# Kernel tuning notes

Hardware: AMD Instinct MI355X
Metric: run time of the kernel (lower is better)

## Reference

```python
import jax, jax.numpy as jnp
import numpy as np

N = 100000          # nodes
E = 1600000         # edges
D_IN = 128
HID = 256
N_CLASSES = 10
N_GRAPHS = 64


def gcn_conv(x, src, dst, W, b, n_nodes):
    """PyG GCNConv: add self-loops, symmetric deg^{-1/2} normalization, x@W, scatter-add."""
    h = x @ W  # [N, out]
    loop = jnp.arange(n_nodes, dtype=src.dtype)
    src2 = jnp.concatenate([src, loop])
    dst2 = jnp.concatenate([dst, loop])
    deg = jax.ops.segment_sum(jnp.ones(src2.shape[0], x.dtype), dst2, num_segments=n_nodes)
    dinv = jax.lax.rsqrt(deg)  # deg >= 1 thanks to self-loops
    norm = dinv[src2] * dinv[dst2]  # [E+N]
    msg = norm[:, None] * h[src2]   # [E+N, out]
    return jax.ops.segment_sum(msg, dst2, num_segments=n_nodes) + b


def setup_inputs() -> dict:
    key = jax.random.key(0)
    ks = jax.random.split(key, 12)
    x = jax.random.normal(ks[0], (N, D_IN), dtype=jnp.float32)
    edge_index = jax.random.randint(ks[1], (2, E), 0, N, dtype=jnp.int64)
    batch = jnp.sort(jax.random.randint(ks[2], (N,), 0, N_GRAPHS, dtype=jnp.int64))
    def glorot(k, shape):
        lim = float(np.sqrt(6.0 / (shape[0] + shape[1])))
        return jax.random.uniform(k, shape, jnp.float32, -lim, lim)
    W1 = glorot(ks[3], (D_IN, HID));  b1 = jnp.zeros((HID,), jnp.float32)
    W2 = glorot(ks[4], (HID, HID));   b2 = jnp.zeros((HID,), jnp.float32)
    Wf1 = glorot(ks[5], (HID, HID));  bf1 = jnp.zeros((HID,), jnp.float32)
    Wf2 = glorot(ks[6], (HID, N_CLASSES)); bf2 = jnp.zeros((N_CLASSES,), jnp.float32)
    return {"x": x, "edge_index": edge_index, "batch": batch,
            "W1": W1, "b1": b1, "W2": W2, "b2": b2,
            "Wf1": Wf1, "bf1": bf1, "Wf2": Wf2, "bf2": bf2}


def reference(x, edge_index, batch, W1, b1, W2, b2, Wf1, bf1, Wf2, bf2):
    src, dst = edge_index[0], edge_index[1]
    h = jax.nn.relu(gcn_conv(x, src, dst, W1, b1, N))
    h = jax.nn.relu(gcn_conv(h, src, dst, W2, b2, N))
    # global mean pool over graph ids
    summed = jax.ops.segment_sum(h, batch, num_segments=N_GRAPHS)  # [G, HID]
    counts = jax.ops.segment_sum(jnp.ones((N,), h.dtype), batch, num_segments=N_GRAPHS)
    pooled = summed / jnp.maximum(counts, 1.0)[:, None]
    z = jax.nn.relu(pooled @ Wf1 + bf1)
    alpha = jax.nn.softplus(z @ Wf2 + bf2) + 0.001
    return alpha
```

## Files before the change

kernel.cpp:

```cpp
#include <hip/hip_runtime.h>
#include <math.h>

#define NN   100000
#define NE   1600000
#define DIN  128
#define HID  256
#define NG   64
#define NCLS 10

#define NBLK 128
#define EPB  (NE / NBLK)
#define NBUK 512
#define NPB  196

using bf16x8 = __attribute__((ext_vector_type(8))) short;
using f32x4  = __attribute__((ext_vector_type(4))) float;
using f32x2  = __attribute__((ext_vector_type(2))) float;
using u32x2  = __attribute__((ext_vector_type(2))) unsigned int;

static __device__ __forceinline__ unsigned short f2bf(float f) {
    unsigned u = __float_as_uint(f);
    u += 0x7fff + ((u >> 16) & 1);
    return (unsigned short)(u >> 16);
}
static __device__ __forceinline__ float bf2f(unsigned short h) {
    return __uint_as_float(((unsigned)h) << 16);
}

static __device__ __forceinline__ unsigned char f32_to_fp8(float f) {
    float a = fminf(fabsf(f), 448.f);
    unsigned bits = __float_as_uint(a * 0x1p-120f);
    bits += 0x7ffff + ((bits >> 20) & 1);
    unsigned e4 = (bits >> 20) & 0x7f;
    return (unsigned char)(e4 | (f < 0.f ? 0x80u : 0u));
}
#if __has_builtin(__builtin_amdgcn_cvt_pk_f32_fp8)
#define HAVE_CVT_FP8 1
#endif
static __device__ __forceinline__ void fp8x4_to_f32(unsigned u, float* f) {
#ifdef HAVE_CVT_FP8
    f32x2 lo = __builtin_amdgcn_cvt_pk_f32_fp8((int)u, false);
    f32x2 hi = __builtin_amdgcn_cvt_pk_f32_fp8((int)u, true);
    f[0] = lo[0]; f[1] = lo[1]; f[2] = hi[0]; f[3] = hi[1];
#else
#pragma unroll
    for (int k = 0; k < 4; ++k) {
        unsigned b = (u >> (8 * k)) & 0xffu;
        unsigned bits = ((b & 0x80u) << 24) | ((b & 0x7fu) << 20);
        f[k] = __uint_as_float(bits) * 0x1p+120f;
    }
#endif
}


__global__ __launch_bounds__(256) void k_hist(const int* __restrict__ dst,
                                              int* __restrict__ histg) {
    __shared__ int h[NBUK];
    const int t = threadIdx.x;
    for (int i = t; i < NBUK; i += 256) h[i] = 0;
    __syncthreads();
    const int e0 = blockIdx.x * EPB, e1 = e0 + EPB;
    for (int e = e0 + t; e < e1; e += 256)
        atomicAdd(&h[(unsigned)__builtin_nontemporal_load(&dst[e]) / NPB], 1);
    __syncthreads();
    for (int i = t; i < NBUK; i += 256)
        histg[i * NBLK + blockIdx.x] = h[i];
}

__global__ __launch_bounds__(1024) void k_scan64k(int* __restrict__ d) {
    __shared__ int ts[1024];
    const int t = threadIdx.x;
    const int base = t * 64;
    int s = 0;
    for (int i = 0; i < 64; ++i) s += d[base + i];
    ts[t] = s;
    __syncthreads();
    for (int off = 1; off < 1024; off <<= 1) {
        int u = (t >= off) ? ts[t - off] : 0;
        __syncthreads();
        ts[t] += u;
        __syncthreads();
    }
    int run = ts[t] - s;
    for (int i = 0; i < 64; ++i) {
        int v = d[base + i];
        d[base + i] = run;
        run += v;
    }
}

__global__ __launch_bounds__(256) void k_scatter(const int* __restrict__ src,
                                                 const int* __restrict__ dst,
                                                 const int* __restrict__ offg,
                                                 int2* __restrict__ pairs) {
    __shared__ int cur[NBUK];
    const int t = threadIdx.x;
    for (int i = t; i < NBUK; i += 256) cur[i] = offg[i * NBLK + blockIdx.x];
    __syncthreads();
    const int e0 = blockIdx.x * EPB, e1 = e0 + EPB;
    for (int e = e0 + t; e < e1; e += 256) {
        int d = __builtin_nontemporal_load(&dst[e]);
        int sv = __builtin_nontemporal_load(&src[e]);
        int b = (unsigned)d / NPB;
        int p = atomicAdd(&cur[b], 1);
        u32x2 pv; pv.x = (unsigned)sv; pv.y = (unsigned)d;
        __builtin_nontemporal_store(pv, (u32x2*)&pairs[p]);
    }
}

__global__ __launch_bounds__(256) void k_csr(const int2* __restrict__ pairs,
                                             const int* __restrict__ offg,
                                             int* __restrict__ csr,
                                             int* __restrict__ deg,
                                             float* __restrict__ dinv,
                                             int* __restrict__ offs) {
    __shared__ int cnt[NPB];
    __shared__ int loff[256];
    __shared__ int cur[NPB];
    const int b = blockIdx.x, t = threadIdx.x;
    const int s     = offg[b * NBLK];
    const int e_end = (b == NBUK - 1) ? NE : offg[(b + 1) * NBLK];
    const int nb0   = b * NPB;
    const int nnod  = min(NPB, NN - nb0);
    if (t < NPB) cnt[t] = 0;
    __syncthreads();
    for (int e = s + t; e < e_end; e += 256)
        atomicAdd(&cnt[pairs[e].y - nb0], 1);
    __syncthreads();
    int v = (t < NPB) ? cnt[t] : 0;
    loff[t] = v;
    __syncthreads();
    for (int off = 1; off < 256; off <<= 1) {
        int u = (t >= off) ? loff[t - off] : 0;
        __syncthreads();
        loff[t] += u;
        __syncthreads();
    }
    int myoff = loff[t] - v;
    __syncthreads();
    loff[t] = myoff;
    if (t < NPB) cur[t] = 0;
    __syncthreads();
    if (t < nnod) {
        int node = nb0 + t;
        int dg = cnt[t];
        deg[node]  = dg;
        dinv[node] = rsqrtf((float)(dg + 1));
        offs[node] = s + myoff;
    }
    for (int e = s + t; e < e_end; e += 256) {
        int2 pr = pairs[e];
        int li = pr.y - nb0;
        int p = atomicAdd(&cur[li], 1);
        csr[s + loff[li] + p] = pr.x;
    }
}

__global__ void k_counts(const int* __restrict__ batch, float* __restrict__ countsf) {
    int g = threadIdx.x;
    if (g >= NG) return;
    int lo = 0, hi = NN;
    while (lo < hi) { int mid = (lo + hi) >> 1; if (batch[mid] < g) lo = mid + 1; else hi = mid; }
    int lb = lo;
    lo = 0; hi = NN;
    while (lo < hi) { int mid = (lo + hi) >> 1; if (batch[mid] <= g) lo = mid + 1; else hi = mid; }
    countsf[g] = (float)(lo - lb);
}


__global__ void k_cast_scale_x(const float* __restrict__ x, const float* __restrict__ dinv,
                               unsigned short* __restrict__ xb, int n4) {
    int i = blockIdx.x * blockDim.x + threadIdx.x;
    if (i >= n4) return;
    float dv = dinv[i >> 5];
    const float4 v = *(const float4*)&x[i * 4];
    ushort4 o;
    o.x = f2bf(v.x * dv); o.y = f2bf(v.y * dv);
    o.z = f2bf(v.z * dv); o.w = f2bf(v.w * dv);
    *(ushort4*)&xb[i * 4] = o;
}

__global__ void k_cast_wt2(const float* __restrict__ W1, unsigned short* __restrict__ Wt1,
                           const float* __restrict__ W2, unsigned short* __restrict__ Wt2) {
    int i = blockIdx.x * blockDim.x + threadIdx.x;
    if (i < DIN * HID) {
        int k = i >> 8, nc = i & 255;
        Wt1[nc * DIN + k] = f2bf(W1[i]);
    } else if (i < (DIN + HID) * HID) {
        int j = i - DIN * HID;
        int k = j >> 8, nc = j & 255;
        Wt2[nc * HID + k] = f2bf(W2[j]);
    }
}


template <int MODE>
__global__ __launch_bounds__(256) void k_gemm_mfma(const unsigned short* __restrict__ A,
                                                   const unsigned short* __restrict__ Wt,
                                                   const float* __restrict__ dinv,
                                                   const float* __restrict__ bias,
                                                   void* __restrict__ outp,
                                                   const int* __restrict__ batch,
                                                   float* __restrict__ pooled,
                                                   int M, int K) {
    __shared__ unsigned short As[128 * 40];
    __shared__ unsigned short Bs[128 * 40];
    __shared__ float psum[4][128];
    __shared__ int gloc[128];
    const int t = threadIdx.x;
    const int lane = t & 63;
    const int wid = t >> 6;
    const int wr = wid >> 1, wc = wid & 1;
    const int bm = blockIdx.x * 128, bn = blockIdx.y * 128;
    const int lr = lane & 15;
    const int ko = (lane >> 4) << 3;

    f32x4 acc[4][4] = {};

    const int r = t >> 2;
    const int kq = (t & 3) << 3;

    int g0 = 0;
    if (MODE == 2) {
        g0 = batch[bm];
        for (int i = t; i < 4 * 128; i += 256) ((float*)psum)[i] = 0.f;
        if (t < 128) gloc[t] = (bm + t < M) ? (batch[bm + t] - g0) : 0;
    }

    for (int kk = 0; kk < K; kk += 32) {
#pragma unroll
        for (int h = 0; h < 128; h += 64) {
            int row = bm + r + h;
            int4 v = make_int4(0, 0, 0, 0);
            if (row < M) v = *(const int4*)&A[(size_t)row * K + kk + kq];
            *(int4*)&As[(r + h) * 40 + kq] = v;
        }
#pragma unroll
        for (int h = 0; h < 128; h += 64) {
            int nrow = bn + r + h;
            int4 v = *(const int4*)&Wt[(size_t)nrow * K + kk + kq];
            *(int4*)&Bs[(r + h) * 40 + kq] = v;
        }
        __syncthreads();
        bf16x8 af[4], bfr[4];
#pragma unroll
        for (int mf = 0; mf < 4; ++mf)
            af[mf] = *(const bf16x8*)&As[(wr * 64 + mf * 16 + lr) * 40 + ko];
#pragma unroll
        for (int nf = 0; nf < 4; ++nf)
            bfr[nf] = *(const bf16x8*)&Bs[(wc * 64 + nf * 16 + lr) * 40 + ko];
#pragma unroll
        for (int mf = 0; mf < 4; ++mf)
#pragma unroll
            for (int nf = 0; nf < 4; ++nf)
                acc[mf][nf] = __builtin_amdgcn_mfma_f32_16x16x32_bf16(af[mf], bfr[nf], acc[mf][nf], 0, 0, 0);
        __syncthreads();
    }

    if (MODE == 1) {
        unsigned char* out8 = (unsigned char*)outp;
#pragma unroll
        for (int mf = 0; mf < 4; ++mf) {
#pragma unroll
            for (int b = 0; b < 4; ++b) {
                int row = bm + wr * 64 + mf * 16 + (lane >> 4) * 4 + b;
                if (row >= M) continue;
                float dv = dinv[row];
#pragma unroll
                for (int nf = 0; nf < 4; ++nf) {
                    int col = bn + wc * 64 + nf * 16 + lr;
                    float v = fmaxf(acc[mf][nf][b] + bias[col], 0.f);
                    out8[(size_t)row * HID + col] = f32_to_fp8(dv * v);
                }
            }
        }
    } else {
        const int q4 = (lane >> 4) << 2;
#pragma unroll
        for (int nf = 0; nf < 4; ++nf) {
            const int lcol = wc * 64 + nf * 16 + lr;
            const float bb = bias[bn + lcol];
            float run = 0.f; int gcur = 0;
#pragma unroll
            for (int mf = 0; mf < 4; ++mf) {
#pragma unroll
                for (int b = 0; b < 4; ++b) {
                    int lrow = wr * 64 + mf * 16 + q4 + b;
                    if (bm + lrow < M) {
                        int gl = gloc[lrow];
                        float v = fmaxf(acc[mf][nf][b] + bb, 0.f);
                        if (gl != gcur) {
                            if (run != 0.f) {
                                if (gcur < 4) atomicAdd(&psum[gcur][lcol], run);
                                else atomicAdd(&pooled[(size_t)(g0 + gcur) * HID + bn + lcol], run);
                            }
                            run = 0.f; gcur = gl;
                        }
                        run += v;
                    }
                }
            }
            if (run != 0.f) {
                if (gcur < 4) atomicAdd(&psum[gcur][lcol], run);
                else atomicAdd(&pooled[(size_t)(g0 + gcur) * HID + bn + lcol], run);
            }
        }
        __syncthreads();
        for (int i = t; i < 4 * 128; i += 256) {
            int gl = i >> 7, lcol = i & 127;
            int g = g0 + gl;
            float v = psum[gl][lcol];
            if (g < NG && v != 0.f)
                atomicAdd(&pooled[(size_t)g * HID + bn + lcol], v);
        }
    }
}


__global__ __launch_bounds__(256) void k_agg256(const unsigned char* __restrict__ hs,
                                                const int* __restrict__ csr,
                                                const int* __restrict__ offs,
                                                const int* __restrict__ deg,
                                                const float* __restrict__ dinv,
                                                unsigned short* __restrict__ out, int n) {
    int wid = threadIdx.x >> 6, lane = threadIdx.x & 63;
    int node = blockIdx.x * 4 + wid;
    if (node >= n) return;
    int c = lane << 2;
    float a0, a1, a2, a3;
    {
        unsigned u = *(const unsigned*)&hs[(size_t)node * HID + c];
        float f[4]; fp8x4_to_f32(u, f);
        a0 = f[0]; a1 = f[1]; a2 = f[2]; a3 = f[3];
    }
    int s0 = offs[node], cnt = deg[node];
    for (int base = 0; base < cnt; base += 64) {
        int nb = min(64, cnt - base);
        int idx = (lane < nb) ? __builtin_nontemporal_load(&csr[s0 + base + lane]) : 0;
        int i = 0;
        for (; i + 8 <= nb; i += 8) {
            unsigned v[8];
#pragma unroll
            for (int k = 0; k < 8; ++k) {
                int j = __shfl(idx, i + k);
                v[k] = *(const unsigned*)&hs[(size_t)j * HID + c];
            }
#pragma unroll
            for (int k = 0; k < 8; ++k) {
                float f[4]; fp8x4_to_f32(v[k], f);
                a0 += f[0]; a1 += f[1]; a2 += f[2]; a3 += f[3];
            }
        }
        for (; i + 4 <= nb; i += 4) {
            unsigned v[4];
#pragma unroll
            for (int k = 0; k < 4; ++k) {
                int j = __shfl(idx, i + k);
                v[k] = *(const unsigned*)&hs[(size_t)j * HID + c];
            }
#pragma unroll
            for (int k = 0; k < 4; ++k) {
                float f[4]; fp8x4_to_f32(v[k], f);
                a0 += f[0]; a1 += f[1]; a2 += f[2]; a3 += f[3];
            }
        }
        for (; i < nb; ++i) {
            int j = __shfl(idx, i);
            unsigned u = *(const unsigned*)&hs[(size_t)j * HID + c];
            float f[4]; fp8x4_to_f32(u, f);
            a0 += f[0]; a1 += f[1]; a2 += f[2]; a3 += f[3];
        }
    }
    float dv = dinv[node];
    ushort4 r;
    r.x = f2bf(dv * a0); r.y = f2bf(dv * a1);
    r.z = f2bf(dv * a2); r.w = f2bf(dv * a3);
    *(ushort4*)&out[(size_t)node * HID + c] = r;
}


__global__ __launch_bounds__(256) void k_agg128(const unsigned short* __restrict__ xs,
                                                const int* __restrict__ csr,
                                                const int* __restrict__ offs,
                                                const int* __restrict__ deg,
                                                const float* __restrict__ dinv,
                                                unsigned short* __restrict__ out, int n) {
    int wid = threadIdx.x >> 6, lane = threadIdx.x & 63;
    int node = blockIdx.x * 4 + wid;
    if (node >= n) return;
    int half = lane >> 5, l32 = lane & 31;
    int c = l32 << 2;
    float a0 = 0.f, a1 = 0.f, a2 = 0.f, a3 = 0.f;
    if (half == 0) {
        const ushort4 s = *(const ushort4*)&xs[(size_t)node * DIN + c];
        a0 = bf2f(s.x); a1 = bf2f(s.y); a2 = bf2f(s.z); a3 = bf2f(s.w);
    }
    int s0 = offs[node], cnt = deg[node];
    for (int base = 0; base < cnt; base += 64) {
        int nb = min(64, cnt - base);
        int idx = (lane < nb) ? __builtin_nontemporal_load(&csr[s0 + base + lane]) : 0;
        int i = 0;
        for (; i + 8 <= nb; i += 8) {
            ushort4 v[4];
#pragma unroll
            for (int k = 0; k < 4; ++k) {
                int j = __shfl(idx, i + 2 * k + half);
                v[k] = *(const ushort4*)&xs[(size_t)j * DIN + c];
            }
#pragma unroll
            for (int k = 0; k < 4; ++k) {
                a0 += bf2f(v[k].x); a1 += bf2f(v[k].y);
                a2 += bf2f(v[k].z); a3 += bf2f(v[k].w);
            }
        }
        for (; i < nb; i += 2) {
            int e = i + half;
            int j = __shfl(idx, e < nb ? e : 0);
            if (e < nb) {
                const ushort4 v = *(const ushort4*)&xs[(size_t)j * DIN + c];
                a0 += bf2f(v.x); a1 += bf2f(v.y); a2 += bf2f(v.z); a3 += bf2f(v.w);
            }
        }
    }
    a0 += __shfl_xor(a0, 32);
    a1 += __shfl_xor(a1, 32);
    a2 += __shfl_xor(a2, 32);
    a3 += __shfl_xor(a3, 32);
    if (half == 0) {
        float dv = dinv[node];
        ushort4 r;
        r.x = f2bf(dv * a0); r.y = f2bf(dv * a1);
        r.z = f2bf(dv * a2); r.w = f2bf(dv * a3);
        *(ushort4*)&out[(size_t)node * DIN + c] = r;
    }
}


__global__ __launch_bounds__(256) void k_mlp(const float* __restrict__ pooled,
                                             const float* __restrict__ countsf,
                                             const float* __restrict__ Wf1,
                                             const float* __restrict__ bf1,
                                             const float* __restrict__ Wf2,
                                             const float* __restrict__ bf2,
                                             float* __restrict__ out) {
    __shared__ float p[HID];
    __shared__ float z[HID];
    int g = blockIdx.x, t = threadIdx.x;
    float cnt = fmaxf(countsf[g], 1.0f);
    p[t] = pooled[g * HID + t] / cnt;
    __syncthreads();
    float accz = bf1[t];
    for (int k = 0; k < HID; ++k)
        accz = fmaf(p[k], Wf1[k * HID + t], accz);
    z[t] = fmaxf(accz, 0.f);
    __syncthreads();
    if (t < NCLS) {
        float o = bf2[t];
        for (int k = 0; k < HID; ++k)
            o = fmaf(z[k], Wf2[k * NCLS + t], o);
        float sp = fmaxf(o, 0.f) + log1pf(expf(-fabsf(o)));
        out[g * NCLS + t] = sp + 0.001f;
    }
}


extern "C" void kernel_launch(void* const* d_in, const int* in_sizes, int n_in,
                              void* d_out, int out_size, void* d_ws, size_t ws_size,
                              hipStream_t stream) {
    const float* x     = (const float*)d_in[0];
    const int*   ei    = (const int*)d_in[1];
    const int*   batch = (const int*)d_in[2];
    const float* W1    = (const float*)d_in[3];
    const float* b1    = (const float*)d_in[4];
    const float* W2    = (const float*)d_in[5];
    const float* b2    = (const float*)d_in[6];
    const float* Wf1   = (const float*)d_in[7];
    const float* bf1   = (const float*)d_in[8];
    const float* Wf2   = (const float*)d_in[9];
    const float* bf2   = (const float*)d_in[10];
    float* out = (float*)d_out;

    const int* srcv = ei;
    const int* dstv = ei + NE;

    char* p = (char*)d_ws;
    auto take = [&](size_t bytes) -> char* {
        char* q = p; p += (bytes + 255) & ~(size_t)255; return q;
    };
    unsigned short* big0 = (unsigned short*)take((size_t)NN * HID * 2);
    unsigned short* big1 = (unsigned short*)take((size_t)NN * HID * 2);
    unsigned short* xs = big0;
    unsigned short* xa = big0 + (size_t)NN * DIN;
    unsigned char*  h8 = (unsigned char*)big1;
    unsigned short* rB = big0;
    int2* pairs = (int2*)big1;
    unsigned short* wt1  = (unsigned short*)take((size_t)DIN * HID * 2);
    unsigned short* wt2  = (unsigned short*)take((size_t)HID * HID * 2);
    int*   histg   = (int*)take((size_t)NBUK * NBLK * 4);
    int*   deg     = (int*)take((size_t)NN * 4);
    int*   offs    = (int*)take((size_t)NN * 4);
    int*   csr     = (int*)take((size_t)NE * 4);
    float* dinv    = (float*)take((size_t)NN * 4);
    float* pooled  = (float*)take((size_t)NG * HID * 4);
    float* countsf = (float*)take((size_t)NG * 4);

    hipMemsetAsync(pooled, 0, (size_t)NG * HID * 4, stream);

    k_hist<<<NBLK, 256, 0, stream>>>(dstv, histg);
    k_scan64k<<<1, 1024, 0, stream>>>(histg);
    k_scatter<<<NBLK, 256, 0, stream>>>(srcv, dstv, histg, pairs);
    k_csr<<<NBUK, 256, 0, stream>>>(pairs, histg, csr, deg, dinv, offs);
    k_counts<<<1, 64, 0, stream>>>(batch, countsf);

    k_cast_scale_x<<<(NN * DIN / 4 + 255) / 256, 256, 0, stream>>>(x, dinv, xs, NN * DIN / 4);
    k_cast_wt2<<<((DIN + HID) * HID + 255) / 256, 256, 0, stream>>>(W1, wt1, W2, wt2);

    dim3 gg((NN + 127) / 128, HID / 128);
    k_agg128<<<(NN + 3) / 4, 256, 0, stream>>>(xs, csr, offs, deg, dinv, xa, NN);
    k_gemm_mfma<1><<<gg, 256, 0, stream>>>(xa, wt1, dinv, b1, (void*)h8, batch, pooled, NN, DIN);
    k_agg256<<<(NN + 3) / 4, 256, 0, stream>>>(h8, csr, offs, deg, dinv, rB, NN);
    k_gemm_mfma<2><<<gg, 256, 0, stream>>>(rB, wt2, dinv, b2, nullptr, batch, pooled, NN, HID);

    k_mlp<<<NG, 256, 0, stream>>>(pooled, countsf, Wf1, bf1, Wf2, bf2, out);
}
```

Measured before the change: 381.8 us.

## Slice node features into column planes for cache-friendly aggregation gathers

Stores fp8 node features in 8 column planes (16 or 32 bytes per node) and launches aggregation blocks per plane so random neighbour gathers work on a much smaller, cache-resident array. The layer-1 input is also quantized to fp8 instead of bf16 to shrink gather traffic. The GEMM epilogue writes the hidden fp8 output in the planar layout. This trades 8x redundant CSR index reads and narrower per-thread loads, and adds fp8 precision loss on the input, for better L2 hit rates.

Result: slower. 525.7 us (+37.7%).

```diff
diff --git a/kernel.cpp b/kernel.cpp
--- a/kernel.cpp
+++ b/kernel.cpp
@@ -168,16 +168,18 @@
 }
 
 
-__global__ void k_cast_scale_x(const float* __restrict__ x, const float* __restrict__ dinv,
-                               unsigned short* __restrict__ xb, int n4) {
+__global__ void k_cast_x8(const float* __restrict__ x, const float* __restrict__ dinv,
+                          unsigned char* __restrict__ xs8, int nq) {
     int i = blockIdx.x * blockDim.x + threadIdx.x;
-    if (i >= n4) return;
-    float dv = dinv[i >> 5];
-    const float4 v = *(const float4*)&x[i * 4];
-    ushort4 o;
-    o.x = f2bf(v.x * dv); o.y = f2bf(v.y * dv);
-    o.z = f2bf(v.z * dv); o.w = f2bf(v.w * dv);
-    *(ushort4*)&xb[i * 4] = o;
+    if (i >= nq) return;
+    int nd = i >> 5;
+    int q  = i & 31;
+    float dv = dinv[nd];
+    const float4 v = *(const float4*)&x[(size_t)nd * DIN + q * 4];
+    uchar4 o;
+    o.x = f32_to_fp8(v.x * dv); o.y = f32_to_fp8(v.y * dv);
+    o.z = f32_to_fp8(v.z * dv); o.w = f32_to_fp8(v.w * dv);
+    *(uchar4*)&xs8[(size_t)(q >> 2) * NN * 16 + (size_t)nd * 16 + (q & 3) * 4] = o;
 }
 
 __global__ void k_cast_wt2(const float* __restrict__ W1, unsigned short* __restrict__ Wt1,
@@ -270,7 +272,8 @@
                 for (int nf = 0; nf < 4; ++nf) {
                     int col = bn + wc * 64 + nf * 16 + lr;
                     float v = fmaxf(acc[mf][nf][b] + bias[col], 0.f);
-                    out8[(size_t)row * HID + col] = f32_to_fp8(dv * v);
+                    out8[(size_t)(col >> 5) * NN * 32 + (size_t)row * 32 + (col & 31)] =
+                        f32_to_fp8(dv * v);
                 }
             }
         }
@@ -317,122 +320,100 @@
 }
 
 
-__global__ __launch_bounds__(256) void k_agg256(const unsigned char* __restrict__ hs,
-                                                const int* __restrict__ csr,
-                                                const int* __restrict__ offs,
-                                                const int* __restrict__ deg,
-                                                const float* __restrict__ dinv,
-                                                unsigned short* __restrict__ out, int n) {
-    int wid = threadIdx.x >> 6, lane = threadIdx.x & 63;
-    int node = blockIdx.x * 4 + wid;
+__global__ __launch_bounds__(256) void k_agg256s(const unsigned char* __restrict__ h8,
+                                                 const int* __restrict__ csr,
+                                                 const int* __restrict__ offs,
+                                                 const int* __restrict__ deg,
+                                                 const float* __restrict__ dinv,
+                                                 unsigned short* __restrict__ out, int n) {
+    const int s = blockIdx.x & 7, grp = blockIdx.x >> 3;
+    const int t = threadIdx.x;
+    const int node = grp * 32 + (t >> 3);
     if (node >= n) return;
-    int c = lane << 2;
+    const int sub = t & 7;
+    const int c4 = sub * 4;
+    const int lane = t & 63;
+    const int lb = lane & ~7;
+    const unsigned char* plane = h8 + (size_t)s * NN * 32;
+
     float a0, a1, a2, a3;
     {
-        unsigned u = *(const unsigned*)&hs[(size_t)node * HID + c];
+        unsigned u = *(const unsigned*)&plane[(size_t)node * 32 + c4];
         float f[4]; fp8x4_to_f32(u, f);
         a0 = f[0]; a1 = f[1]; a2 = f[2]; a3 = f[3];
     }
-    int s0 = offs[node], cnt = deg[node];
-    for (int base = 0; base < cnt; base += 64) {
-        int nb = min(64, cnt - base);
-        int idx = (lane < nb) ? __builtin_nontemporal_load(&csr[s0 + base + lane]) : 0;
-        int i = 0;
-        for (; i + 8 <= nb; i += 8) {
-            unsigned v[8];
-#pragma unroll
-            for (int k = 0; k < 8; ++k) {
-                int j = __shfl(idx, i + k);
-                v[k] = *(const unsigned*)&hs[(size_t)j * HID + c];
-            }
-#pragma unroll
-            for (int k = 0; k < 8; ++k) {
-                float f[4]; fp8x4_to_f32(v[k], f);
+    const int s0 = offs[node], cnt = deg[node];
+    for (int base = 0; base < cnt; base += 8) {
+        int ia = (base + sub < cnt) ? __builtin_nontemporal_load(&csr[s0 + base + sub]) : 0;
+        int nb = cnt - base; if (nb > 8) nb = 8;
+        unsigned vv[8];
+#pragma unroll
+        for (int k = 0; k < 8; ++k)
+            if (k < nb) {
+                int j = __shfl(ia, lb + k);
+                vv[k] = *(const unsigned*)&plane[(size_t)j * 32 + c4];
+            }
+#pragma unroll
+        for (int k = 0; k < 8; ++k)
+            if (k < nb) {
+                float f[4]; fp8x4_to_f32(vv[k], f);
                 a0 += f[0]; a1 += f[1]; a2 += f[2]; a3 += f[3];
             }
-        }
-        for (; i + 4 <= nb; i += 4) {
-            unsigned v[4];
-#pragma unroll
-            for (int k = 0; k < 4; ++k) {
-                int j = __shfl(idx, i + k);
-                v[k] = *(const unsigned*)&hs[(size_t)j * HID + c];
-            }
-#pragma unroll
-            for (int k = 0; k < 4; ++k) {
-                float f[4]; fp8x4_to_f32(v[k], f);
-                a0 += f[0]; a1 += f[1]; a2 += f[2]; a3 += f[3];
-            }
-        }
-        for (; i < nb; ++i) {
-            int j = __shfl(idx, i);
-            unsigned u = *(const unsigned*)&hs[(size_t)j * HID + c];
-            float f[4]; fp8x4_to_f32(u, f);
-            a0 += f[0]; a1 += f[1]; a2 += f[2]; a3 += f[3];
-        }
     }
     float dv = dinv[node];
     ushort4 r;
     r.x = f2bf(dv * a0); r.y = f2bf(dv * a1);
     r.z = f2bf(dv * a2); r.w = f2bf(dv * a3);
-    *(ushort4*)&out[(size_t)node * HID + c] = r;
-}
-
-
-__global__ __launch_bounds__(256) void k_agg128(const unsigned short* __restrict__ xs,
-                                                const int* __restrict__ csr,
-                                                const int* __restrict__ offs,
-                                                const int* __restrict__ deg,
-                                                const float* __restrict__ dinv,
-                                                unsigned short* __restrict__ out, int n) {
-    int wid = threadIdx.x >> 6, lane = threadIdx.x & 63;
-    int node = blockIdx.x * 4 + wid;
+    *(ushort4*)&out[(size_t)node * HID + s * 32 + c4] = r;
+}
+
+
+__global__ __launch_bounds__(256) void k_agg128s(const unsigned char* __restrict__ xs8,
+                                                 const int* __restrict__ csr,
+                                                 const int* __restrict__ offs,
+                                                 const int* __restrict__ deg,
+                                                 const float* __restrict__ dinv,
+                                                 unsigned short* __restrict__ out, int n) {
+    const int s = blockIdx.x & 7, grp = blockIdx.x >> 3;
+    const int t = threadIdx.x;
+    const int node = grp * 64 + (t >> 2);
     if (node >= n) return;
-    int half = lane >> 5, l32 = lane & 31;
-    int c = l32 << 2;
-    float a0 = 0.f, a1 = 0.f, a2 = 0.f, a3 = 0.f;
-    if (half == 0) {
-        const ushort4 s = *(const ushort4*)&xs[(size_t)node * DIN + c];
-        a0 = bf2f(s.x); a1 = bf2f(s.y); a2 = bf2f(s.z); a3 = bf2f(s.w);
-    }
-    int s0 = offs[node], cnt = deg[node];
-    for (int base = 0; base < cnt; base += 64) {
-        int nb = min(64, cnt - base);
-        int idx = (lane < nb) ? __builtin_nontemporal_load(&csr[s0 + base + lane]) : 0;
-        int i = 0;
-        for (; i + 8 <= nb; i += 8) {
-            ushort4 v[4];
-#pragma unroll
-            for (int k = 0; k < 4; ++k) {
-                int j = __shfl(idx, i + 2 * k + half);
-                v[k] = *(const ushort4*)&xs[(size_t)j * DIN + c];
-            }
-#pragma unroll
-            for (int k = 0; k < 4; ++k) {
-                a0 += bf2f(v[k].x); a1 += bf2f(v[k].y);
-                a2 += bf2f(v[k].z); a3 += bf2f(v[k].w);
-            }
-        }
-        for (; i < nb; i += 2) {
-            int e = i + half;
-            int j = __shfl(idx, e < nb ? e : 0);
-            if (e < nb) {
-                const ushort4 v = *(const ushort4*)&xs[(size_t)j * DIN + c];
-                a0 += bf2f(v.x); a1 += bf2f(v.y); a2 += bf2f(v.z); a3 += bf2f(v.w);
-            }
-        }
-    }
-    a0 += __shfl_xor(a0, 32);
-    a1 += __shfl_xor(a1, 32);
-    a2 += __shfl_xor(a2, 32);
-    a3 += __shfl_xor(a3, 32);
-    if (half == 0) {
-        float dv = dinv[node];
-        ushort4 r;
-        r.x = f2bf(dv * a0); r.y = f2bf(dv * a1);
-        r.z = f2bf(dv * a2); r.w = f2bf(dv * a3);
-        *(ushort4*)&out[(size_t)node * DIN + c] = r;
-    }
+    const int sub = t & 3;
+    const int c4 = sub * 4;
+    const int lane = t & 63;
+    const int lb = lane & ~3;
+    const unsigned char* plane = xs8 + (size_t)s * NN * 16;
+
+    float a0, a1, a2, a3;
+    {
+        unsigned u = *(const unsigned*)&plane[(size_t)node * 16 + c4];
+        float f[4]; fp8x4_to_f32(u, f);
+        a0 = f[0]; a1 = f[1]; a2 = f[2]; a3 = f[3];
+    }
+    const int s0 = offs[node], cnt = deg[node];
+    for (int base = 0; base < cnt; base += 8) {
+        int ia = (base + sub < cnt) ? __builtin_nontemporal_load(&csr[s0 + base + sub]) : 0;
+        int ib = (base + 4 + sub < cnt) ? __builtin_nontemporal_load(&csr[s0 + base + 4 + sub]) : 0;
+        int nb = cnt - base; if (nb > 8) nb = 8;
+        unsigned vv[8];
+#pragma unroll
+        for (int k = 0; k < 8; ++k)
+            if (k < nb) {
+                int j = (k < 4) ? __shfl(ia, lb + k) : __shfl(ib, lb + k - 4);
+                vv[k] = *(const unsigned*)&plane[(size_t)j * 16 + c4];
+            }
+#pragma unroll
+        for (int k = 0; k < 8; ++k)
+            if (k < nb) {
+                float f[4]; fp8x4_to_f32(vv[k], f);
+                a0 += f[0]; a1 += f[1]; a2 += f[2]; a3 += f[3];
+            }
+    }
+    float dv = dinv[node];
+    ushort4 r;
+    r.x = f2bf(dv * a0); r.y = f2bf(dv * a1);
+    r.z = f2bf(dv * a2); r.w = f2bf(dv * a3);
+    *(ushort4*)&out[(size_t)node * DIN + s * 16 + c4] = r;
 }
 
 
@@ -487,12 +468,12 @@
     auto take = [&](size_t bytes) -> char* {
         char* q = p; p += (bytes + 255) & ~(size_t)255; return q;
     };
-    unsigned short* big0 = (unsigned short*)take((size_t)NN * HID * 2);
-    unsigned short* big1 = (unsigned short*)take((size_t)NN * HID * 2);
-    unsigned short* xs = big0;
-    unsigned short* xa = big0 + (size_t)NN * DIN;
-    unsigned char*  h8 = (unsigned char*)big1;
-    unsigned short* rB = big0;
+    char* big0 = take((size_t)NN * HID * 2);
+    char* big1 = take((size_t)NN * HID * 2);
+    unsigned char*  xs8 = (unsigned char*)big0;
+    unsigned short* xa  = (unsigned short*)(big0 + (size_t)NN * 16 * 8);
+    unsigned char*  h8  = (unsigned char*)big1;
+    unsigned short* rB  = (unsigned short*)big0;
     int2* pairs = (int2*)big1;
     unsigned short* wt1  = (unsigned short*)take((size_t)DIN * HID * 2);
     unsigned short* wt2  = (unsigned short*)take((size_t)HID * HID * 2);
@@ -512,13 +493,15 @@
     k_csr<<<NBUK, 256, 0, stream>>>(pairs, histg, csr, deg, dinv, offs);
     k_counts<<<1, 64, 0, stream>>>(batch, countsf);
 
-    k_cast_scale_x<<<(NN * DIN / 4 + 255) / 256, 256, 0, stream>>>(x, dinv, xs, NN * DIN / 4);
+    k_cast_x8<<<(NN * 32 + 255) / 256, 256, 0, stream>>>(x, dinv, xs8, NN * 32);
     k_cast_wt2<<<((DIN + HID) * HID + 255) / 256, 256, 0, stream>>>(W1, wt1, W2, wt2);
 
     dim3 gg((NN + 127) / 128, HID / 128);
-    k_agg128<<<(NN + 3) / 4, 256, 0, stream>>>(xs, csr, offs, deg, dinv, xa, NN);
+    int g128 = ((NN + 63) / 64) * 8;
+    k_agg128s<<<g128, 256, 0, stream>>>(xs8, csr, offs, deg, dinv, xa, NN);
     k_gemm_mfma<1><<<gg, 256, 0, stream>>>(xa, wt1, dinv, b1, (void*)h8, batch, pooled, NN, DIN);
-    k_agg256<<<(NN + 3) / 4, 256, 0, stream>>>(h8, csr, offs, deg, dinv, rB, NN);
+    int g256 = ((NN + 31) / 32) * 8;
+    k_agg256s<<<g256, 256, 0, stream>>>(h8, csr, offs, deg, dinv, rB, NN);
     k_gemm_mfma<2><<<gg, 256, 0, stream>>>(rB, wt2, dinv, b2, nullptr, batch, pooled, NN, HID);
 
     k_mlp<<<NG, 256, 0, stream>>>(pooled, countsf, Wf1, bf1, Wf2, bf2, out);
```
